# Kernel tuning notes

Measured on AMD Instinct MI355X. Metric: run time of the kernel, lower is better.

Reference implementation:

```python
import jax, jax.numpy as jnp
import numpy as np

H = 8
HD = 64
RHO = 0.1


def setup_inputs() -> dict:
    key = jax.random.key(0)
    ks = jax.random.split(key, 5)
    B, L, D = 4, 512, 512
    x = jax.random.normal(ks[0], (B, L, D), dtype=jnp.float32)
    # store projection weights as [in, out] so y = x @ W (equivalent to torch Linear with W.T)
    Wq = jax.random.normal(ks[1], (D, H * HD), dtype=jnp.float32) * 0.02
    Wk = jax.random.normal(ks[2], (D, H * HD), dtype=jnp.float32) * 0.02
    Wv = jax.random.normal(ks[3], (D, H * HD), dtype=jnp.float32) * 0.02
    Wo = jax.random.normal(ks[4], (H * HD, D), dtype=jnp.float32) * 0.02
    return {"x": x, "Wq": Wq, "Wk": Wk, "Wv": Wv, "Wo": Wo}


def _build_adjacency(S):
    # S: [B, H, L, L]. A = (1/L) sum_j [thresholded outer(S[:,:,:,j]) / HD with zero diag]
    B, Hn, L, _ = S.shape
    eye = jnp.eye(L, dtype=bool)
    S_cols = jnp.transpose(S, (3, 0, 1, 2))  # [L, B, H, L]

    def step(acc, s_col):
        # s_col: [B, H, L]; U_j[i,k] = s_col[i] * s_col[k] / HD
        U = s_col[..., :, None] * s_col[..., None, :] / HD  # [B,H,L,L]
        U = jnp.where(eye, 0.0, U)
        A_j = jnp.where(U > RHO, U, 0.0)
        return acc + A_j, None

    A_sum, _ = jax.lax.scan(step, jnp.zeros_like(S), S_cols)
    return A_sum / L


def _normalize_adjacency(A):
    L = A.shape[-1]
    A_tilde = A + jnp.eye(L, dtype=A.dtype)
    D = jnp.clip(A_tilde.sum(axis=-1, keepdims=True), 1e-6, None)
    D_inv_sqrt = D ** -0.5  # [B,H,L,1]
    return D_inv_sqrt * A_tilde * jnp.swapaxes(D_inv_sqrt, -1, -2)


def reference(x, Wq, Wk, Wv, Wo):
    B, L, D = x.shape
    scale = jnp.sqrt(jnp.asarray(HD, dtype=x.dtype))
    def proj(W):
        return jnp.einsum('bld,de->ble', x, W).reshape(B, L, H, HD).transpose(0, 2, 1, 3)
    Q, K, V = proj(Wq), proj(Wk), proj(Wv)  # [B,H,L,HD]
    S = jnp.einsum('bhid,bhjd->bhij', Q, K)  # [B,H,L,L]
    A = _build_adjacency(S)
    A_hat = _normalize_adjacency(A)
    # jump: Phi(S) = A_hat @ S @ A_hat^T
    S_jump = jnp.einsum('bhij,bhjk,bhlk->bhil', A_hat, S, A_hat) / scale
    attn = jax.nn.softmax(S_jump, axis=-1)
    out = jnp.einsum('bhij,bhjd->bhid', attn, V)  # [B,H,L,HD]
    out = out.transpose(0, 2, 1, 3).reshape(B, L, H * HD)
    return jnp.einsum('ble,ed->bld', out, Wo)
```

## Files before the change

### kernel.cpp

```cpp
#include <hip/hip_runtime.h>
#include <math.h>


typedef __attribute__((ext_vector_type(8))) short short8v;
typedef __attribute__((ext_vector_type(4))) float f32x4;
typedef _Float16 h2 __attribute__((ext_vector_type(2)));

__device__ __forceinline__ void split8(const float* v, unsigned* hi, unsigned* lo)
{
    #pragma unroll
    for (int q = 0; q < 4; ++q) {
        const unsigned b0 = __float_as_uint(v[2 * q])     & 0xFFFF0000u;
        const unsigned b1 = __float_as_uint(v[2 * q + 1]) & 0xFFFF0000u;
        const float d0 = v[2 * q]     - __uint_as_float(b0);
        const float d1 = v[2 * q + 1] - __uint_as_float(b1);
        hi[q] = (b0 >> 16) | b1;
        lo[q] = (__float_as_uint(d0) >> 16) | (__float_as_uint(d1) & 0xFFFF0000u);
    }
}

template<int BT, int BN>
__global__ __launch_bounds__(256)
void gemm_mfma(const float* __restrict__ Ap, const float* __restrict__ Bp,
               float* __restrict__ Cp, int K, int lda, int ldb, int ldc,
               long sA, long sB, long sC, float scale)
{
    const float* __restrict__ A = Ap + (long)blockIdx.z * sA;
    const float* __restrict__ B = Bp + (long)blockIdx.z * sB;
    float* __restrict__ C = Cp + (long)blockIdx.z * sC;
    const int m0 = blockIdx.y << 7, n0 = blockIdx.x * BN;
    constexpr int NF = BN / 32;

    __shared__ short Ah[128 * 32], Al[128 * 32];
    __shared__ short Bh[BN * 32], Bl[BN * 32];

    const int tid = threadIdx.x;
    const int lane = tid & 63, wv = tid >> 6;
    const int wr = wv >> 1, wc = wv & 1;

    f32x4 acc[4][NF] = {};

    for (int k0 = 0; k0 < K; k0 += 32) {
        {
            const int row = tid >> 1;
            const int swz = (row & 3) ^ ((row >> 2) & 3);
            #pragma unroll
            for (int gg = 0; gg < 2; ++gg) {
                const int g = ((tid & 1) << 1) + gg;
                const float* src = A + (long)(m0 + row) * lda + k0 + (g << 3);
                float v[8];
                *(float4*)&v[0] = *(const float4*)src;
                *(float4*)&v[4] = *(const float4*)(src + 4);
                unsigned hi[4], lo[4];
                split8(v, hi, lo);
                const int off = row * 32 + ((g ^ swz) << 3);
                *(uint4*)&Ah[off] = *(uint4*)hi;
                *(uint4*)&Al[off] = *(uint4*)lo;
            }
        }
        if (BT) {
            if (BN == 128) {
                const int row = tid >> 1;
                const int swz = (row & 3) ^ ((row >> 2) & 3);
                #pragma unroll
                for (int gg = 0; gg < 2; ++gg) {
                    const int g = ((tid & 1) << 1) + gg;
                    const float* src = B + (long)(n0 + row) * ldb + k0 + (g << 3);
                    float v[8];
                    *(float4*)&v[0] = *(const float4*)src;
                    *(float4*)&v[4] = *(const float4*)(src + 4);
                    unsigned hi[4], lo[4];
                    split8(v, hi, lo);
                    const int off = row * 32 + ((g ^ swz) << 3);
                    *(uint4*)&Bh[off] = *(uint4*)hi;
                    *(uint4*)&Bl[off] = *(uint4*)lo;
                }
            } else {
                const int row = tid >> 2;
                const int g = tid & 3;
                const int swz = (row & 3) ^ ((row >> 2) & 3);
                const float* src = B + (long)(n0 + row) * ldb + k0 + (g << 3);
                float v[8];
                *(float4*)&v[0] = *(const float4*)src;
                *(float4*)&v[4] = *(const float4*)(src + 4);
                unsigned hi[4], lo[4];
                split8(v, hi, lo);
                const int off = row * 32 + ((g ^ swz) << 3);
                *(uint4*)&Bh[off] = *(uint4*)hi;
                *(uint4*)&Bl[off] = *(uint4*)lo;
            }
        } else {
            if (BN == 128) {
                const int n = tid & 127;
                const int swz = (n & 3) ^ ((n >> 2) & 3);
                #pragma unroll
                for (int gg = 0; gg < 2; ++gg) {
                    const int g = ((tid >> 7) << 1) + gg;
                    float v[8];
                    #pragma unroll
                    for (int e = 0; e < 8; ++e)
                        v[e] = B[(long)(k0 + (g << 3) + e) * ldb + n0 + n];
                    unsigned hi[4], lo[4];
                    split8(v, hi, lo);
                    const int off = n * 32 + ((g ^ swz) << 3);
                    *(uint4*)&Bh[off] = *(uint4*)hi;
                    *(uint4*)&Bl[off] = *(uint4*)lo;
                }
            } else {
                const int n = tid & 63;
                const int g = tid >> 6;
                const int swz = (n & 3) ^ ((n >> 2) & 3);
                float v[8];
                #pragma unroll
                for (int e = 0; e < 8; ++e)
                    v[e] = B[(long)(k0 + (g << 3) + e) * ldb + n0 + n];
                unsigned hi[4], lo[4];
                split8(v, hi, lo);
                const int off = n * 32 + ((g ^ swz) << 3);
                *(uint4*)&Bh[off] = *(uint4*)hi;
                *(uint4*)&Bl[off] = *(uint4*)lo;
            }
        }
        __syncthreads();

        {
            const int r = lane & 15, g = lane >> 4;
            const int lswz = (r & 3) ^ ((r >> 2) & 3);
            const int gslot = ((g ^ lswz) << 3);
            const int abase = ((wr << 6) + r) * 32 + gslot;
            const int bbase = (wc * (BN >> 1) + r) * 32 + gslot;
            short8v afh[4], afl[4], bfh[NF], bfl[NF];
            #pragma unroll
            for (int f = 0; f < 4; ++f) {
                afh[f] = *(short8v*)&Ah[abase + f * 512];
                afl[f] = *(short8v*)&Al[abase + f * 512];
            }
            #pragma unroll
            for (int f = 0; f < NF; ++f) {
                bfh[f] = *(short8v*)&Bh[bbase + f * 512];
                bfl[f] = *(short8v*)&Bl[bbase + f * 512];
            }
            #pragma unroll
            for (int fi = 0; fi < 4; ++fi)
                #pragma unroll
                for (int fj = 0; fj < NF; ++fj) {
                    acc[fi][fj] = __builtin_amdgcn_mfma_f32_16x16x32_bf16(
                        afh[fi], bfh[fj], acc[fi][fj], 0, 0, 0);
                    acc[fi][fj] = __builtin_amdgcn_mfma_f32_16x16x32_bf16(
                        afh[fi], bfl[fj], acc[fi][fj], 0, 0, 0);
                    acc[fi][fj] = __builtin_amdgcn_mfma_f32_16x16x32_bf16(
                        afl[fi], bfh[fj], acc[fi][fj], 0, 0, 0);
                }
        }
        __syncthreads();
    }

    const int r = lane & 15, g = lane >> 4;
    #pragma unroll
    for (int fi = 0; fi < 4; ++fi) {
        const int gr0 = m0 + (wr << 6) + fi * 16 + g * 4;
        #pragma unroll
        for (int fj = 0; fj < NF; ++fj) {
            const int gc = n0 + wc * (BN >> 1) + fj * 16 + r;
            #pragma unroll
            for (int qq = 0; qq < 4; ++qq)
                C[(long)(gr0 + qq) * ldc + gc] = acc[fi][fj][qq] * scale;
        }
    }
}

__global__ __launch_bounds__(256)
void gemm_qkv_mfma(const float* __restrict__ x, const float* __restrict__ Wq,
                   const float* __restrict__ Wk, const float* __restrict__ Wv,
                   float* __restrict__ QKV)
{
    const int m0 = blockIdx.y << 7;
    const int ng = blockIdx.x << 7;
    const float* __restrict__ W = (ng < 512) ? Wq : (ng < 1024) ? Wk : Wv;
    const int n0 = ng & 511;
    float* __restrict__ C = QKV + (long)(ng >> 9) * (1 << 20);

    __shared__ short Ah[128 * 32], Al[128 * 32], Bh[128 * 32], Bl[128 * 32];

    const int tid = threadIdx.x;
    const int lane = tid & 63, wv = tid >> 6;
    const int wr = wv >> 1, wc = wv & 1;

    f32x4 acc[4][4] = {};

    for (int k0 = 0; k0 < 512; k0 += 32) {
        {
            const int row = tid >> 1;
            const int swz = (row & 3) ^ ((row >> 2) & 3);
            #pragma unroll
            for (int gg = 0; gg < 2; ++gg) {
                const int g = ((tid & 1) << 1) + gg;
                const float* src = x + (long)(m0 + row) * 512 + k0 + (g << 3);
                float v[8];
                *(float4*)&v[0] = *(const float4*)src;
                *(float4*)&v[4] = *(const float4*)(src + 4);
                unsigned hi[4], lo[4];
                split8(v, hi, lo);
                const int off = row * 32 + ((g ^ swz) << 3);
                *(uint4*)&Ah[off] = *(uint4*)hi;
                *(uint4*)&Al[off] = *(uint4*)lo;
            }
        }
        {
            const int n = tid & 127;
            const int swz = (n & 3) ^ ((n >> 2) & 3);
            #pragma unroll
            for (int gg = 0; gg < 2; ++gg) {
                const int g = ((tid >> 7) << 1) + gg;
                float v[8];
                #pragma unroll
                for (int e = 0; e < 8; ++e)
                    v[e] = W[(long)(k0 + (g << 3) + e) * 512 + n0 + n];
                unsigned hi[4], lo[4];
                split8(v, hi, lo);
                const int off = n * 32 + ((g ^ swz) << 3);
                *(uint4*)&Bh[off] = *(uint4*)hi;
                *(uint4*)&Bl[off] = *(uint4*)lo;
            }
        }
        __syncthreads();

        {
            const int r = lane & 15, g = lane >> 4;
            const int lswz = (r & 3) ^ ((r >> 2) & 3);
            const int gslot = ((g ^ lswz) << 3);
            const int abase = ((wr << 6) + r) * 32 + gslot;
            const int bbase = ((wc << 6) + r) * 32 + gslot;
            short8v afh[4], afl[4], bfh[4], bfl[4];
            #pragma unroll
            for (int f = 0; f < 4; ++f) {
                afh[f] = *(short8v*)&Ah[abase + f * 512];
                afl[f] = *(short8v*)&Al[abase + f * 512];
                bfh[f] = *(short8v*)&Bh[bbase + f * 512];
                bfl[f] = *(short8v*)&Bl[bbase + f * 512];
            }
            #pragma unroll
            for (int fi = 0; fi < 4; ++fi)
                #pragma unroll
                for (int fj = 0; fj < 4; ++fj) {
                    acc[fi][fj] = __builtin_amdgcn_mfma_f32_16x16x32_bf16(
                        afh[fi], bfh[fj], acc[fi][fj], 0, 0, 0);
                    acc[fi][fj] = __builtin_amdgcn_mfma_f32_16x16x32_bf16(
                        afh[fi], bfl[fj], acc[fi][fj], 0, 0, 0);
                    acc[fi][fj] = __builtin_amdgcn_mfma_f32_16x16x32_bf16(
                        afl[fi], bfh[fj], acc[fi][fj], 0, 0, 0);
                }
        }
        __syncthreads();
    }

    const int r = lane & 15, g = lane >> 4;
    #pragma unroll
    for (int fi = 0; fi < 4; ++fi) {
        const int gr0 = m0 + (wr << 6) + fi * 16 + g * 4;
        #pragma unroll
        for (int fj = 0; fj < 4; ++fj) {
            const int nl = n0 + (wc << 6) + fj * 16 + r;
            const int h = nl >> 6, d = nl & 63;
            #pragma unroll
            for (int qq = 0; qq < 4; ++qq) {
                const int m = gr0 + qq;
                const int b = m >> 9, l = m & 511;
                C[((long)((b * 8 + h) * 512 + l)) * 64 + d] = acc[fi][fj][qq];
            }
        }
    }
}

__global__ __launch_bounds__(256, 4)
void adj_kernel(const float* __restrict__ S, float* __restrict__ P0,
                float* __restrict__ P1)
{
    const int bh = blockIdx.z;
    const float* __restrict__ Sh = S + (long)bh * 262144;
    float* __restrict__ Ph = ((blockIdx.y == 0) ? P0 : P1) + (long)bh * 262144;
    const int jbase = blockIdx.y << 8;

    int ti = 0, rem = blockIdx.x;
    while (rem >= 8 - ti) { rem -= 8 - ti; ++ti; }
    const int tk = ti + rem;
    const int i0 = ti << 6, k0 = tk << 6;

    __shared__ __align__(16) char smem_raw[17408];

    const int tid  = threadIdx.x;
    const int lane = tid & 63;
    const int wv   = tid >> 6;
    const int ly8  = (lane >> 3) << 3;
    const int lx8  = (lane & 7) << 3;
    const int r4   = lane >> 2;
    const int q    = lane & 3;

    h2 (*stgL)[68] = (h2(*)[68])(smem_raw + wv * 4352);
    h2 (*stgR)[68] = (h2(*)[68])(smem_raw + wv * 4352 + 2176);

    const h2 nC2  = { (_Float16)(-6.4f), (_Float16)(-6.4f) };
    const h2 z2   = { (_Float16)0.0f,    (_Float16)0.0f };
    const h2 big2 = { (_Float16)32768.0f,(_Float16)32768.0f };
    const h2 c2   = { (_Float16)6.4f,    (_Float16)6.4f };

    h2 acc2[8][8];
    #pragma unroll
    for (int i = 0; i < 8; ++i)
        #pragma unroll
        for (int j = 0; j < 8; ++j)
            acc2[i][j] = z2;

    const int jw = jbase + (wv << 6);
    const float* srcL = Sh + (long)(i0 + r4) * 512 + jw + (q << 2);
    const float* srcR = Sh + (long)(k0 + r4) * 512 + jw + (q << 2);

    float4 rl[4], rr[4];
    #pragma unroll
    for (int p = 0; p < 4; ++p) {
        rl[p] = *(const float4*)(srcL + (long)(p << 4) * 512);
        rr[p] = *(const float4*)(srcR + (long)(p << 4) * 512);
    }

    for (int c = 0; c < 4; ++c) {
        #pragma unroll
        for (int p = 0; p < 4; ++p) {
            const int row = r4 + (p << 4);
            h2 h0, h1;
            h0[0] = (_Float16)rl[p].x; h0[1] = (_Float16)rl[p].y;
            h1[0] = (_Float16)rl[p].z; h1[1] = (_Float16)rl[p].w;
            stgL[(q << 1) + 0][row] = h0;
            stgL[(q << 1) + 1][row] = h1;
            h0[0] = (_Float16)rr[p].x; h0[1] = (_Float16)rr[p].y;
            h1[0] = (_Float16)rr[p].z; h1[1] = (_Float16)rr[p].w;
            stgR[(q << 1) + 0][row] = h0;
            stgR[(q << 1) + 1][row] = h1;
        }
        if (c < 3) {
            const int joff = (c + 1) << 4;
            #pragma unroll
            for (int p = 0; p < 4; ++p) {
                rl[p] = *(const float4*)(srcL + (long)(p << 4) * 512 + joff);
                rr[p] = *(const float4*)(srcR + (long)(p << 4) * 512 + joff);
            }
        }
        asm volatile("s_waitcnt lgkmcnt(0)" ::: "memory");
        __builtin_amdgcn_sched_barrier(0);
        #pragma unroll
        for (int jp = 0; jp < 8; ++jp) {
            h2 a2[8], b2[8];
            *(uint4*)&a2[0] = *(const uint4*)&stgL[jp][ly8];
            *(uint4*)&a2[4] = *(const uint4*)&stgL[jp][ly8 + 4];
            *(uint4*)&b2[0] = *(const uint4*)&stgR[jp][lx8];
            *(uint4*)&b2[4] = *(const uint4*)&stgR[jp][lx8 + 4];
            #pragma unroll
            for (int i = 0; i < 8; ++i)
                #pragma unroll
                for (int j = 0; j < 8; ++j) {
                    const h2 d = a2[i] * b2[j] + nC2;
                    const h2 t = __builtin_elementwise_max(d, z2);
                    const h2 m = __builtin_elementwise_min(t * big2 + t, t + c2);
                    acc2[i][j] += m;
                }
        }
    }

    float* buf0 = (float*)smem_raw;
    float* buf1 = (float*)(smem_raw + 4352);
    float  f[8][8];

    #pragma unroll
    for (int qp = 0; qp < 4; ++qp) {
        float v[16];
        #pragma unroll
        for (int e = 0; e < 16; ++e) {
            const h2 hh = acc2[(qp << 1) + (e >> 3)][e & 7];
            v[e] = (float)hh[0] + (float)hh[1];
        }
        __syncthreads();
        if (wv == 1 || wv == 2) {
            float* dst = (wv == 1 ? buf0 : buf1) + lane * 17;
            #pragma unroll
            for (int e = 0; e < 16; ++e) dst[e] = v[e];
        }
        __syncthreads();
        if (wv == 0 || wv == 3) {
            const float* src = (wv == 0 ? buf0 : buf1) + lane * 17;
            #pragma unroll
            for (int e = 0; e < 16; ++e) v[e] += src[e];
        }
        __syncthreads();
        if (wv == 3) {
            float* dst = buf0 + lane * 17;
            #pragma unroll
            for (int e = 0; e < 16; ++e) dst[e] = v[e];
        }
        __syncthreads();
        if (wv == 0) {
            const float* src = buf0 + lane * 17;
            #pragma unroll
            for (int e = 0; e < 16; ++e)
                f[(qp << 1) + (e >> 3)][e & 7] = v[e] + src[e];
        }
    }

    if (wv == 0) {
        const float SC = 1.0f / 32768.0f;
        #pragma unroll
        for (int i = 0; i < 8; ++i)
            #pragma unroll
            for (int j = 0; j < 8; ++j)
                f[i][j] *= SC;
        if (ti == tk) {
            #pragma unroll
            for (int i = 0; i < 8; ++i)
                #pragma unroll
                for (int j = 0; j < 8; ++j)
                    if (ly8 + i == lx8 + j) f[i][j] = 0.0f;
        }
        #pragma unroll
        for (int i = 0; i < 8; ++i) {
            float* dst = Ph + (long)(i0 + ly8 + i) * 512 + k0 + lx8;
            *(float4*)dst       = make_float4(f[i][0], f[i][1], f[i][2], f[i][3]);
            *(float4*)(dst + 4) = make_float4(f[i][4], f[i][5], f[i][6], f[i][7]);
        }
        if (ti != tk) {
            #pragma unroll
            for (int j = 0; j < 8; ++j) {
                float* dst = Ph + (long)(k0 + lx8 + j) * 512 + i0 + ly8;
                *(float4*)dst       = make_float4(f[0][j], f[1][j], f[2][j], f[3][j]);
                *(float4*)(dst + 4) = make_float4(f[4][j], f[5][j], f[6][j], f[7][j]);
            }
        }
    }
}

__global__ __launch_bounds__(256)
void rowsum_kernel(const float* __restrict__ P0, const float* __restrict__ P1,
                   float* __restrict__ R)
{
    const int row = (blockIdx.x << 2) + (threadIdx.x >> 6);
    const int lane = threadIdx.x & 63;
    const float* p0 = P0 + (long)row * 512;
    const float* p1 = P1 + (long)row * 512;
    float s = 0.0f;
    #pragma unroll
    for (int t = 0; t < 8; ++t) s += p0[lane + (t << 6)] + p1[lane + (t << 6)];
    #pragma unroll
    for (int off = 32; off; off >>= 1) s += __shfl_xor(s, off, 64);
    if (lane == 0) R[row] = 1.0f / sqrtf(fmaxf(1.0f + s, 1e-6f));
}

__global__ __launch_bounds__(256)
void ahat_kernel(float* __restrict__ P0, const float* __restrict__ P1,
                 const float* __restrict__ R)
{
    const long i4 = ((long)blockIdx.x * 256 + threadIdx.x) << 2;
    const long off = i4 & 262143;
    const long bh = i4 >> 18;
    const int i = (int)(off >> 9);
    const int k = (int)(off & 511);
    const float ri = R[(bh << 9) + i];
    const float* Rk = R + (bh << 9) + k;
    float4 v0 = *(float4*)(P0 + i4);
    float4 v1 = *(const float4*)(P1 + i4);
    v0.x = ri * Rk[0] * ((v0.x + v1.x) + ((k + 0) == i ? 1.0f : 0.0f));
    v0.y = ri * Rk[1] * ((v0.y + v1.y) + ((k + 1) == i ? 1.0f : 0.0f));
    v0.z = ri * Rk[2] * ((v0.z + v1.z) + ((k + 2) == i ? 1.0f : 0.0f));
    v0.w = ri * Rk[3] * ((v0.w + v1.w) + ((k + 3) == i ? 1.0f : 0.0f));
    *(float4*)(P0 + i4) = v0;
}

__global__ __launch_bounds__(256)
void softmax_kernel(float* __restrict__ P)
{
    const int row = (blockIdx.x << 2) + (threadIdx.x >> 6);
    const int lane = threadIdx.x & 63;
    float* p = P + (long)row * 512 + (lane << 3);
    float4 v0 = *(float4*)p;
    float4 v1 = *(float4*)(p + 4);
    float mx = fmaxf(fmaxf(fmaxf(v0.x, v0.y), fmaxf(v0.z, v0.w)),
                     fmaxf(fmaxf(v1.x, v1.y), fmaxf(v1.z, v1.w)));
    #pragma unroll
    for (int off = 32; off; off >>= 1) mx = fmaxf(mx, __shfl_xor(mx, off, 64));
    float e[8];
    e[0] = __expf(v0.x - mx); e[1] = __expf(v0.y - mx);
    e[2] = __expf(v0.z - mx); e[3] = __expf(v0.w - mx);
    e[4] = __expf(v1.x - mx); e[5] = __expf(v1.y - mx);
    e[6] = __expf(v1.z - mx); e[7] = __expf(v1.w - mx);
    float s = (((e[0] + e[1]) + (e[2] + e[3])) + ((e[4] + e[5]) + (e[6] + e[7])));
    #pragma unroll
    for (int off = 32; off; off >>= 1) s += __shfl_xor(s, off, 64);
    const float inv = 1.0f / s;
    *(float4*)p       = make_float4(e[0] * inv, e[1] * inv, e[2] * inv, e[3] * inv);
    *(float4*)(p + 4) = make_float4(e[4] * inv, e[5] * inv, e[6] * inv, e[7] * inv);
}

__global__ __launch_bounds__(256)
void gemm_pv_mfma(const float* __restrict__ P, const float* __restrict__ V,
                  float* __restrict__ Of)
{
    const int bh = blockIdx.z;
    const float* __restrict__ Pp = P + (long)bh * 262144;
    const float* __restrict__ Vp = V + (long)bh * 32768;
    const int bb = bh >> 3, hh = bh & 7;
    const int m0 = blockIdx.y << 7;

    __shared__ short Ph[128 * 32], Pl[128 * 32], Vh[64 * 32], Vl[64 * 32];

    const int tid = threadIdx.x;
    const int lane = tid & 63, wv = tid >> 6;

    f32x4 acc[2][4] = {};

    for (int k0 = 0; k0 < 512; k0 += 32) {
        {
            const int row = tid >> 1;
            const int swz = (row & 3) ^ ((row >> 2) & 3);
            #pragma unroll
            for (int gg = 0; gg < 2; ++gg) {
                const int g = ((tid & 1) << 1) + gg;
                const float* src = Pp + (long)(m0 + row) * 512 + k0 + (g << 3);
                float v[8];
                *(float4*)&v[0] = *(const float4*)src;
                *(float4*)&v[4] = *(const float4*)(src + 4);
                unsigned hi[4], lo[4];
                split8(v, hi, lo);
                const int off = row * 32 + ((g ^ swz) << 3);
                *(uint4*)&Ph[off] = *(uint4*)hi;
                *(uint4*)&Pl[off] = *(uint4*)lo;
            }
        }
        {
            const int n = tid & 63, g = tid >> 6;
            const int swz = (n & 3) ^ ((n >> 2) & 3);
            float v[8];
            #pragma unroll
            for (int e = 0; e < 8; ++e)
                v[e] = Vp[(long)(k0 + (g << 3) + e) * 64 + n];
            unsigned hi[4], lo[4];
            split8(v, hi, lo);
            const int off = n * 32 + ((g ^ swz) << 3);
            *(uint4*)&Vh[off] = *(uint4*)hi;
            *(uint4*)&Vl[off] = *(uint4*)lo;
        }
        __syncthreads();

        {
            const int r = lane & 15, g = lane >> 4;
            const int lswz = (r & 3) ^ ((r >> 2) & 3);
            const int gslot = ((g ^ lswz) << 3);
            short8v afh[2], afl[2], bfh[4], bfl[4];
            #pragma unroll
            for (int fi = 0; fi < 2; ++fi) {
                const int abase = ((wv << 5) + (fi << 4) + r) * 32 + gslot;
                afh[fi] = *(short8v*)&Ph[abase];
                afl[fi] = *(short8v*)&Pl[abase];
            }
            #pragma unroll
            for (int fj = 0; fj < 4; ++fj) {
                const int bbase = ((fj << 4) + r) * 32 + gslot;
                bfh[fj] = *(short8v*)&Vh[bbase];
                bfl[fj] = *(short8v*)&Vl[bbase];
            }
            #pragma unroll
            for (int fi = 0; fi < 2; ++fi)
                #pragma unroll
                for (int fj = 0; fj < 4; ++fj) {
                    acc[fi][fj] = __builtin_amdgcn_mfma_f32_16x16x32_bf16(
                        afh[fi], bfh[fj], acc[fi][fj], 0, 0, 0);
                    acc[fi][fj] = __builtin_amdgcn_mfma_f32_16x16x32_bf16(
                        afh[fi], bfl[fj], acc[fi][fj], 0, 0, 0);
                    acc[fi][fj] = __builtin_amdgcn_mfma_f32_16x16x32_bf16(
                        afl[fi], bfh[fj], acc[fi][fj], 0, 0, 0);
                }
        }
        __syncthreads();
    }

    const int r = lane & 15, g = lane >> 4;
    #pragma unroll
    for (int fi = 0; fi < 2; ++fi) {
        const int l0 = m0 + (wv << 5) + fi * 16 + g * 4;
        #pragma unroll
        for (int fj = 0; fj < 4; ++fj) {
            const int d = fj * 16 + r;
            #pragma unroll
            for (int qq = 0; qq < 4; ++qq)
                Of[((long)((bb << 9) + l0 + qq) << 9) + (hh << 6) + d] = acc[fi][fj][qq];
        }
    }
}

extern "C" void kernel_launch(void* const* d_in, const int* in_sizes, int n_in,
                              void* d_out, int out_size, void* d_ws, size_t ws_size,
                              hipStream_t stream)
{
    const float* x  = (const float*)d_in[0];
    const float* Wq = (const float*)d_in[1];
    const float* Wk = (const float*)d_in[2];
    const float* Wv = (const float*)d_in[3];
    const float* Wo = (const float*)d_in[4];
    float* out = (float*)d_out;

    float* ws = (float*)d_ws;
    float* Q  = ws;
    float* Kt = Q  + (1u << 20);
    float* V  = Kt + (1u << 20);
    float* S  = V  + (1u << 20);
    float* Am = S  + (8u << 20);
    float* T  = Am + (8u << 20);
    float* R  = T  + (8u << 20);

    dim3 blk(256);

    gemm_qkv_mfma<<<dim3(12, 16, 1), blk, 0, stream>>>(x, Wq, Wk, Wv, Q);

    gemm_mfma<1, 128><<<dim3(4, 4, 32), blk, 0, stream>>>(Q, Kt, S, 64, 64, 64, 512,
                                                          32768, 32768, 262144, 1.0f);

    adj_kernel<<<dim3(36, 2, 32), blk, 0, stream>>>(S, Am, T);

    rowsum_kernel<<<dim3(4096), blk, 0, stream>>>(Am, T, R);

    ahat_kernel<<<dim3(8192), blk, 0, stream>>>(Am, T, R);

    gemm_mfma<0, 64><<<dim3(8, 4, 32), blk, 0, stream>>>(Am, S, T, 512, 512, 512, 512,
                                                         262144, 262144, 262144, 1.0f);

    gemm_mfma<1, 64><<<dim3(8, 4, 32), blk, 0, stream>>>(T, Am, S, 512, 512, 512, 512,
                                                         262144, 262144, 262144, 0.125f);

    softmax_kernel<<<dim3(4096), blk, 0, stream>>>(S);

    gemm_pv_mfma<<<dim3(1, 4, 32), blk, 0, stream>>>(S, V, Q);

    gemm_mfma<0, 64><<<dim3(8, 16, 1), blk, 0, stream>>>(Q, Wo, out, 512, 512, 512, 512,
                                                         0, 0, 0, 1.0f);
}
```

Baseline: 435.9 us.

## Use inline packed-f16 asm in adjacency loop and widen GEMM tiles to 128

The adjacency kernel's inner threshold-accumulate loop now runs on raw 32-bit words through explicit v_pk_fma/max/add/min_f16 inline assembly instead of vector-typed f16 arithmetic. This pins down the instruction sequence and stops the compiler from adding extra conversions or splitting the packed ops. Separately, the three 512x512 GEMM launches move from 64-wide to 128-wide column tiles, which halves the grid in x. Larger tiles raise data reuse per block but lower the block count and may raise register pressure.

```diff
diff --git a/kernel.cpp b/kernel.cpp
--- a/kernel.cpp
+++ b/kernel.cpp
@@ -296,20 +296,15 @@
     const int r4   = lane >> 2;
     const int q    = lane & 3;
 
-    h2 (*stgL)[68] = (h2(*)[68])(smem_raw + wv * 4352);
-    h2 (*stgR)[68] = (h2(*)[68])(smem_raw + wv * 4352 + 2176);
-
-    const h2 nC2  = { (_Float16)(-6.4f), (_Float16)(-6.4f) };
-    const h2 z2   = { (_Float16)0.0f,    (_Float16)0.0f };
-    const h2 big2 = { (_Float16)32768.0f,(_Float16)32768.0f };
-    const h2 c2   = { (_Float16)6.4f,    (_Float16)6.4f };
-
-    h2 acc2[8][8];
-    #pragma unroll
-    for (int i = 0; i < 8; ++i)
-        #pragma unroll
-        for (int j = 0; j < 8; ++j)
-            acc2[i][j] = z2;
+    unsigned (*stgL)[68] = (unsigned(*)[68])(smem_raw + wv * 4352);
+    unsigned (*stgR)[68] = (unsigned(*)[68])(smem_raw + wv * 4352 + 2176);
+
+    const unsigned nC  = 0xC666C666u;
+    const unsigned zz  = 0x00000000u;
+    const unsigned big = 0x78007800u;
+    const unsigned cc  = 0x46664666u;
+
+    unsigned acc2[8][8] = {};
 
     const int jw = jbase + (wv << 6);
     const float* srcL = Sh + (long)(i0 + r4) * 512 + jw + (q << 2);
@@ -329,12 +324,12 @@
             h2 h0, h1;
             h0[0] = (_Float16)rl[p].x; h0[1] = (_Float16)rl[p].y;
             h1[0] = (_Float16)rl[p].z; h1[1] = (_Float16)rl[p].w;
-            stgL[(q << 1) + 0][row] = h0;
-            stgL[(q << 1) + 1][row] = h1;
+            stgL[(q << 1) + 0][row] = __builtin_bit_cast(unsigned, h0);
+            stgL[(q << 1) + 1][row] = __builtin_bit_cast(unsigned, h1);
             h0[0] = (_Float16)rr[p].x; h0[1] = (_Float16)rr[p].y;
             h1[0] = (_Float16)rr[p].z; h1[1] = (_Float16)rr[p].w;
-            stgR[(q << 1) + 0][row] = h0;
-            stgR[(q << 1) + 1][row] = h1;
+            stgR[(q << 1) + 0][row] = __builtin_bit_cast(unsigned, h0);
+            stgR[(q << 1) + 1][row] = __builtin_bit_cast(unsigned, h1);
         }
         if (c < 3) {
             const int joff = (c + 1) << 4;
@@ -348,7 +343,7 @@
         __builtin_amdgcn_sched_barrier(0);
         #pragma unroll
         for (int jp = 0; jp < 8; ++jp) {
-            h2 a2[8], b2[8];
+            unsigned a2[8], b2[8];
             *(uint4*)&a2[0] = *(const uint4*)&stgL[jp][ly8];
             *(uint4*)&a2[4] = *(const uint4*)&stgL[jp][ly8 + 4];
             *(uint4*)&b2[0] = *(const uint4*)&stgR[jp][lx8];
@@ -357,10 +352,19 @@
             for (int i = 0; i < 8; ++i)
                 #pragma unroll
                 for (int j = 0; j < 8; ++j) {
-                    const h2 d = a2[i] * b2[j] + nC2;
-                    const h2 t = __builtin_elementwise_max(d, z2);
-                    const h2 m = __builtin_elementwise_min(t * big2 + t, t + c2);
-                    acc2[i][j] += m;
+                    unsigned d, t, m1, m2, m;
+                    asm("v_pk_fma_f16 %0, %1, %2, %3"
+                        : "=v"(d) : "v"(a2[i]), "v"(b2[j]), "v"(nC));
+                    asm("v_pk_max_f16 %0, %1, %2"
+                        : "=v"(t) : "v"(d), "v"(zz));
+                    asm("v_pk_fma_f16 %0, %1, %2, %3"
+                        : "=v"(m1) : "v"(t), "v"(big), "v"(t));
+                    asm("v_pk_add_f16 %0, %1, %2"
+                        : "=v"(m2) : "v"(t), "v"(cc));
+                    asm("v_pk_min_f16 %0, %1, %2"
+                        : "=v"(m) : "v"(m1), "v"(m2));
+                    asm("v_pk_add_f16 %0, %1, %0"
+                        : "+v"(acc2[i][j]) : "v"(m));
                 }
         }
     }
@@ -374,7 +378,7 @@
         float v[16];
         #pragma unroll
         for (int e = 0; e < 16; ++e) {
-            const h2 hh = acc2[(qp << 1) + (e >> 3)][e & 7];
+            const h2 hh = __builtin_bit_cast(h2, acc2[(qp << 1) + (e >> 3)][e & 7]);
             v[e] = (float)hh[0] + (float)hh[1];
         }
         __syncthreads();
@@ -625,16 +629,16 @@
 
     ahat_kernel<<<dim3(8192), blk, 0, stream>>>(Am, T, R);
 
-    gemm_mfma<0, 64><<<dim3(8, 4, 32), blk, 0, stream>>>(Am, S, T, 512, 512, 512, 512,
-                                                         262144, 262144, 262144, 1.0f);
-
-    gemm_mfma<1, 64><<<dim3(8, 4, 32), blk, 0, stream>>>(T, Am, S, 512, 512, 512, 512,
-                                                         262144, 262144, 262144, 0.125f);
+    gemm_mfma<0, 128><<<dim3(4, 4, 32), blk, 0, stream>>>(Am, S, T, 512, 512, 512, 512,
+                                                          262144, 262144, 262144, 1.0f);
+
+    gemm_mfma<1, 128><<<dim3(4, 4, 32), blk, 0, stream>>>(T, Am, S, 512, 512, 512, 512,
+                                                          262144, 262144, 262144, 0.125f);
 
     softmax_kernel<<<dim3(4096), blk, 0, stream>>>(S);
 
     gemm_pv_mfma<<<dim3(1, 4, 32), blk, 0, stream>>>(S, V, Q);
 
-    gemm_mfma<0, 64><<<dim3(8, 16, 1), blk, 0, stream>>>(Q, Wo, out, 512, 512, 512, 512,
-                                                         0, 0, 0, 1.0f);
-}
+    gemm_mfma<0, 128><<<dim3(4, 16, 1), blk, 0, stream>>>(Q, Wo, out, 512, 512, 512, 512,
+                                                          0, 0, 0, 1.0f);
+}
```

New measurement: 416.7 us. -4.4%, faster.
